# Optimization experiments

Hardware: AMD Instinct MI355X
Metric: run time of the kernel (lower is better)

Reference implementation:

```python
import jax, jax.numpy as jnp
import numpy as np

MARGIN = 0.3
EPS = 1e-16


def _pairwise_distances(e):
    # e: [N, D] -> [N, N] euclidean distances (non-squared path)
    dot = jnp.matmul(e, e.T)
    sq = jnp.diagonal(dot)
    d = sq[None, :] + sq[:, None] - 2.0 * dot
    d = jnp.maximum(d, 0.0)
    zmask = (d == 0.0).astype(d.dtype)
    d = jnp.sqrt(d + zmask * EPS) * (1.0 - zmask)
    return d


def _masks(labels):
    n = labels.shape[0]
    eq = labels[None, :] == labels[:, None]          # [N, N]
    not_diag = ~jnp.eye(n, dtype=bool)
    ap_mask = eq & not_diag                          # anchor-positive
    an_mask = ~eq                                    # anchor-negative
    return ap_mask, an_mask


def _hard_loss(e, labels):
    d = _pairwise_distances(e)
    ap_mask, an_mask = _masks(labels)
    apf = ap_mask.astype(d.dtype)
    anf = an_mask.astype(d.dtype)
    hardest_pos = (apf * d).max(axis=1)
    max_d = d.max()
    hardest_neg = (d + max_d * (1.0 - anf)).min(axis=1)
    tl = jax.nn.relu(hardest_pos - hardest_neg + MARGIN)
    valid = apf.sum(axis=1) > 0
    cnt = valid.sum().astype(d.dtype)
    mean_loss = jnp.where(valid, tl, 0.0).sum() / jnp.maximum(cnt, 1.0)
    return jnp.where(cnt > 0, mean_loss, (e * 0).sum())


def _semi_hard_loss(e, labels):
    d = _pairwise_distances(e)                       # [N, N]
    ap_mask, an_mask = _masks(labels)
    ap = d[:, :, None]                               # [N, N, 1] anchor-positive dist
    an = d[:, None, :]                               # [N, 1, N] anchor-negative dist
    loss = ap - an + MARGIN                          # [N, N, N]
    valid = (ap_mask[:, :, None] & an_mask[:, None, :]
             & (an > ap) & (loss > 0))               # [N, N, N] bool
    num_valid = valid.sum()
    semi = (loss * valid.astype(loss.dtype)).sum() / jnp.maximum(
        num_valid.astype(loss.dtype), 1.0)
    return jnp.where(num_valid > 0, semi, _hard_loss(e, labels))


def setup_inputs() -> dict:
    key = jax.random.key(0)
    k1, k2 = jax.random.split(key)
    embeddings = jax.random.normal(k1, (384, 256), dtype=jnp.float32)
    labels = jax.random.randint(k2, (384,), 0, 32, dtype=jnp.int64)
    return {"embeddings": embeddings, "labels": labels}


def reference(embeddings, labels):
    return _semi_hard_loss(embeddings, labels)
```

## Files before the change

kernel.cpp:

```cpp
#include <hip/hip_runtime.h>
#include <math.h>

#define N 384
#define D 256
#define D4 (D/4)
#define A 3
#define GRID (N/A)
#define TPB N
#define NW (TPB/64)
#define MARGIN_F 0.3f

__global__ __launch_bounds__(TPB) void k_rows(const float* __restrict__ e,
                                              const int* __restrict__ labels,
                                              float* __restrict__ semi_sum,
                                              int* __restrict__ semi_cnt,
                                              float* __restrict__ hp_arr,
                                              float* __restrict__ mn_arr,
                                              float* __restrict__ rm_arr,
                                              int* __restrict__ pc_arr) {
  __shared__ float4 ei[A][D4];
  __shared__ float  nrm[N];
  __shared__ float  row[A][N];
  __shared__ float  negd[A][N];
  __shared__ int    lab[N];
  __shared__ int    poslist[A][N];
  __shared__ int    npos[A];
  __shared__ float  wredf[A][4][NW];
  __shared__ int    wredi[A][2][NW];

  const int b = blockIdx.x;
  const int t = threadIdx.x;
  const int i0 = b * A;

  lab[t] = labels[t];
  if (t < A * D4) {
    int a = t / D4, c = t % D4;
    ei[a][c] = ((const float4*)e)[(size_t)(i0 + a) * D4 + c];
  }
  if (t < A) npos[t] = 0;
  __syncthreads();

  const float4* ej = (const float4*)(e + (size_t)t * D);
  float4 dv0 = {0,0,0,0}, dv1 = {0,0,0,0}, dv2 = {0,0,0,0}, nv = {0,0,0,0};
#pragma unroll 8
  for (int c = 0; c < D4; ++c) {
    float4 v = ej[c];
    nv.x += v.x*v.x; nv.y += v.y*v.y; nv.z += v.z*v.z; nv.w += v.w*v.w;
    float4 u0 = ei[0][c];
    dv0.x += u0.x*v.x; dv0.y += u0.y*v.y; dv0.z += u0.z*v.z; dv0.w += u0.w*v.w;
    float4 u1 = ei[1][c];
    dv1.x += u1.x*v.x; dv1.y += u1.y*v.y; dv1.z += u1.z*v.z; dv1.w += u1.w*v.w;
    float4 u2 = ei[2][c];
    dv2.x += u2.x*v.x; dv2.y += u2.y*v.y; dv2.z += u2.z*v.z; dv2.w += u2.w*v.w;
  }
  const float nj = (nv.x + nv.y) + (nv.z + nv.w);
  float dots[A];
  dots[0] = (dv0.x + dv0.y) + (dv0.z + dv0.w);
  dots[1] = (dv1.x + dv1.y) + (dv1.z + dv1.w);
  dots[2] = (dv2.x + dv2.y) + (dv2.z + dv2.w);
  nrm[t] = nj;
  __syncthreads();

  const int lj = lab[t];
  float hpv[A], mnv[A], rmv[A];
  int   pcv[A];
#pragma unroll
  for (int a = 0; a < A; ++a) {
    const float ni = nrm[i0 + a];
    float d2 = fmaxf(ni + nj - 2.0f * dots[a], 0.0f);
    float dvv = (d2 > 0.0f) ? sqrtf(d2) : 0.0f;
    const bool eq    = (lj == lab[i0 + a]);
    const bool ispos = eq && (t != i0 + a);
    row[a][t]  = dvv;
    negd[a][t] = eq ? 1e30f : dvv;
    rmv[a] = dvv;
    mnv[a] = eq ? 1e30f : dvv;
    hpv[a] = ispos ? dvv : 0.0f;
    pcv[a] = ispos ? 1 : 0;
    if (ispos) { int idx = atomicAdd(&npos[a], 1); poslist[a][idx] = t; }
  }
  __syncthreads();

  const int w = t >> 6;
#pragma unroll
  for (int a = 0; a < A; ++a) {
    const float an = negd[a][t];
    float s = 0.0f;
    int   c = 0;
    const int np = npos[a];
    for (int p = 0; p < np; ++p) {
      const float ap = row[a][poslist[a][p]];
      const float loss = ap - an + MARGIN_F;
      if (an > ap && loss > 0.0f) { s += loss; c++; }
    }
    float hp = hpv[a], mn = mnv[a], rm = rmv[a];
    int   pc = pcv[a];
    for (int off = 32; off; off >>= 1) {
      s  += __shfl_down(s, off);
      c  += __shfl_down(c, off);
      hp  = fmaxf(hp, __shfl_down(hp, off));
      mn  = fminf(mn, __shfl_down(mn, off));
      rm  = fmaxf(rm, __shfl_down(rm, off));
      pc += __shfl_down(pc, off);
    }
    if ((t & 63) == 0) {
      wredf[a][0][w] = s;  wredf[a][1][w] = hp;
      wredf[a][2][w] = mn; wredf[a][3][w] = rm;
      wredi[a][0][w] = c;  wredi[a][1][w] = pc;
    }
  }
  __syncthreads();
  if (t < A) {
    float S = 0.0f, HP = 0.0f, MN = 1e30f, RM = 0.0f;
    int   C = 0, PC = 0;
    for (int ww = 0; ww < NW; ++ww) {
      S += wredf[t][0][ww];
      HP = fmaxf(HP, wredf[t][1][ww]);
      MN = fminf(MN, wredf[t][2][ww]);
      RM = fmaxf(RM, wredf[t][3][ww]);
      C += wredi[t][0][ww];
      PC += wredi[t][1][ww];
    }
    const int i = i0 + t;
    semi_sum[i] = S; semi_cnt[i] = C;
    hp_arr[i] = HP;  mn_arr[i] = MN;
    rm_arr[i] = RM;  pc_arr[i] = PC;
  }
}

__global__ __launch_bounds__(N) void k_final(const float* __restrict__ semi_sum,
                                             const int* __restrict__ semi_cnt,
                                             const float* __restrict__ hp_arr,
                                             const float* __restrict__ mn_arr,
                                             const float* __restrict__ rm_arr,
                                             const int* __restrict__ pc_arr,
                                             float* __restrict__ out) {
  const int t = threadIdx.x;
  __shared__ float shf[12];
  __shared__ int   shi[6];
  __shared__ float s_maxd, s_tsum;
  __shared__ int   s_tcnt;

  float s  = semi_sum[t];
  float rm = rm_arr[t];
  int   c  = semi_cnt[t];
  for (int off = 32; off; off >>= 1) {
    s += __shfl_down(s, off);
    rm = fmaxf(rm, __shfl_down(rm, off));
    c += __shfl_down(c, off);
  }
  const int wv = t >> 6;
  if ((t & 63) == 0) { shf[wv] = s; shf[6 + wv] = rm; shi[wv] = c; }
  __syncthreads();
  if (t == 0) {
    float ts = 0.0f, md = 0.0f; int tc = 0;
    for (int w = 0; w < 6; ++w) { ts += shf[w]; md = fmaxf(md, shf[6 + w]); tc += shi[w]; }
    s_tsum = ts; s_tcnt = tc; s_maxd = md;
  }
  __syncthreads();
  const float maxd = s_maxd;

  float hp  = hp_arr[t];
  float mnv = mn_arr[t];
  int   pcv = pc_arr[t];
  float hn  = fminf(mnv, maxd);
  float tl  = fmaxf(hp - hn + MARGIN_F, 0.0f);
  int   vld = (pcv > 0) ? 1 : 0;
  float contrib = vld ? tl : 0.0f;
  for (int off = 32; off; off >>= 1) {
    contrib += __shfl_down(contrib, off);
    vld += __shfl_down(vld, off);
  }
  __syncthreads();
  if ((t & 63) == 0) { shf[wv] = contrib; shi[wv] = vld; }
  __syncthreads();
  if (t == 0) {
    float hs = 0.0f; int vc = 0;
    for (int w = 0; w < 6; ++w) { hs += shf[w]; vc += shi[w]; }
    float semi = s_tsum / fmaxf((float)s_tcnt, 1.0f);
    float hard = (vc > 0) ? (hs / (float)vc) : 0.0f;
    out[0] = (s_tcnt > 0) ? semi : hard;
  }
}

extern "C" void kernel_launch(void* const* d_in, const int* in_sizes, int n_in,
                              void* d_out, int out_size, void* d_ws, size_t ws_size,
                              hipStream_t stream) {
  (void)in_sizes; (void)n_in; (void)out_size; (void)ws_size;
  const float* e      = (const float*)d_in[0];
  const int*   labels = (const int*)d_in[1];
  float*       out    = (float*)d_out;

  float* ws       = (float*)d_ws;
  float* semi_sum = ws;
  float* hp_arr   = ws + N;
  float* mn_arr   = ws + 2 * N;
  float* rm_arr   = ws + 3 * N;
  int*   semi_cnt = (int*)(ws + 4 * N);
  int*   pc_arr   = (int*)(ws + 5 * N);

  k_rows<<<GRID, TPB, 0, stream>>>(e, labels, semi_sum, semi_cnt,
                                   hp_arr, mn_arr, rm_arr, pc_arr);
  k_final<<<1, N, 0, stream>>>(semi_sum, semi_cnt, hp_arr, mn_arr, rm_arr,
                               pc_arr, out);
}
```

Baseline: 75.34 us.

## Coalesce embedding loads via 16-lane cooperative dot products and single-wave final reduce

In the old row kernel each thread streamed its own embedding row with strided float4 loads, so a wave's accesses were uncoalesced across 64 rows. Now 16 lanes cooperate on one row, each reading contiguous float4 chunks, and combine partial norms and dot products with width-16 shuffles before staging them in shared memory. This is meant to improve global-memory coalescing, at the cost of extra shuffles, a shared-memory round trip and one more barrier. The final kernel also drops from six waves to a single wave that reduces with shuffles only, removing its shared-memory and barrier steps.

After: 70.94 us. -5.8%, faster.

```diff
diff --git a/kernel.cpp b/kernel.cpp
--- a/kernel.cpp
+++ b/kernel.cpp
@@ -20,6 +20,7 @@
                                               int* __restrict__ pc_arr) {
   __shared__ float4 ei[A][D4];
   __shared__ float  nrm[N];
+  __shared__ float  sdot[N][A];
   __shared__ float  row[A][N];
   __shared__ float  negd[A][N];
   __shared__ int    lab[N];
@@ -40,28 +41,47 @@
   if (t < A) npos[t] = 0;
   __syncthreads();
 
-  const float4* ej = (const float4*)(e + (size_t)t * D);
-  float4 dv0 = {0,0,0,0}, dv1 = {0,0,0,0}, dv2 = {0,0,0,0}, nv = {0,0,0,0};
-#pragma unroll 8
-  for (int c = 0; c < D4; ++c) {
-    float4 v = ej[c];
-    nv.x += v.x*v.x; nv.y += v.y*v.y; nv.z += v.z*v.z; nv.w += v.w*v.w;
-    float4 u0 = ei[0][c];
-    dv0.x += u0.x*v.x; dv0.y += u0.y*v.y; dv0.z += u0.z*v.z; dv0.w += u0.w*v.w;
-    float4 u1 = ei[1][c];
-    dv1.x += u1.x*v.x; dv1.y += u1.y*v.y; dv1.z += u1.z*v.z; dv1.w += u1.w*v.w;
-    float4 u2 = ei[2][c];
-    dv2.x += u2.x*v.x; dv2.y += u2.y*v.y; dv2.z += u2.z*v.z; dv2.w += u2.w*v.w;
-  }
-  const float nj = (nv.x + nv.y) + (nv.z + nv.w);
+  {
+    const int w   = t >> 6;
+    const int ln  = t & 63;
+    const int r4  = ln >> 4;
+    const int l16 = ln & 15;
+    const float4* e4 = (const float4*)e;
+    for (int p = 0; p < 16; ++p) {
+      const int j = w * 64 + p * 4 + r4;
+      float nj = 0.f, d0 = 0.f, d1 = 0.f, d2 = 0.f;
+#pragma unroll
+      for (int k = 0; k < 4; ++k) {
+        const int c = l16 + k * 16;
+        const float4 v  = e4[(size_t)j * D4 + c];
+        const float4 u0 = ei[0][c];
+        const float4 u1 = ei[1][c];
+        const float4 u2 = ei[2][c];
+        nj += v.x*v.x + v.y*v.y + v.z*v.z + v.w*v.w;
+        d0 += u0.x*v.x + u0.y*v.y + u0.z*v.z + u0.w*v.w;
+        d1 += u1.x*v.x + u1.y*v.y + u1.z*v.z + u1.w*v.w;
+        d2 += u2.x*v.x + u2.y*v.y + u2.z*v.z + u2.w*v.w;
+      }
+#pragma unroll
+      for (int off = 8; off; off >>= 1) {
+        nj += __shfl_down(nj, off, 16);
+        d0 += __shfl_down(d0, off, 16);
+        d1 += __shfl_down(d1, off, 16);
+        d2 += __shfl_down(d2, off, 16);
+      }
+      if (l16 == 0) {
+        nrm[j] = nj;
+        sdot[j][0] = d0; sdot[j][1] = d1; sdot[j][2] = d2;
+      }
+    }
+  }
+  __syncthreads();
+
+  const int lj = lab[t];
+  const float nj = nrm[t];
   float dots[A];
-  dots[0] = (dv0.x + dv0.y) + (dv0.z + dv0.w);
-  dots[1] = (dv1.x + dv1.y) + (dv1.z + dv1.w);
-  dots[2] = (dv2.x + dv2.y) + (dv2.z + dv2.w);
-  nrm[t] = nj;
-  __syncthreads();
-
-  const int lj = lab[t];
+  dots[0] = sdot[t][0]; dots[1] = sdot[t][1]; dots[2] = sdot[t][2];
+
   float hpv[A], mnv[A], rmv[A];
   int   pcv[A];
 #pragma unroll
@@ -128,58 +148,54 @@
   }
 }
 
-__global__ __launch_bounds__(N) void k_final(const float* __restrict__ semi_sum,
-                                             const int* __restrict__ semi_cnt,
-                                             const float* __restrict__ hp_arr,
-                                             const float* __restrict__ mn_arr,
-                                             const float* __restrict__ rm_arr,
-                                             const int* __restrict__ pc_arr,
-                                             float* __restrict__ out) {
+__global__ __launch_bounds__(64) void k_final(const float* __restrict__ semi_sum,
+                                              const int* __restrict__ semi_cnt,
+                                              const float* __restrict__ hp_arr,
+                                              const float* __restrict__ mn_arr,
+                                              const float* __restrict__ rm_arr,
+                                              const int* __restrict__ pc_arr,
+                                              float* __restrict__ out) {
   const int t = threadIdx.x;
-  __shared__ float shf[12];
-  __shared__ int   shi[6];
-  __shared__ float s_maxd, s_tsum;
-  __shared__ int   s_tcnt;
-
-  float s  = semi_sum[t];
-  float rm = rm_arr[t];
-  int   c  = semi_cnt[t];
+
+  float S = 0.0f, RM = 0.0f;
+  int   C = 0;
+#pragma unroll
+  for (int i = 0; i < 6; ++i) {
+    const int r = t + 64 * i;
+    S += semi_sum[r];
+    RM = fmaxf(RM, rm_arr[r]);
+    C += semi_cnt[r];
+  }
   for (int off = 32; off; off >>= 1) {
-    s += __shfl_down(s, off);
-    rm = fmaxf(rm, __shfl_down(rm, off));
-    c += __shfl_down(c, off);
-  }
-  const int wv = t >> 6;
-  if ((t & 63) == 0) { shf[wv] = s; shf[6 + wv] = rm; shi[wv] = c; }
-  __syncthreads();
+    S  += __shfl_down(S, off);
+    RM  = fmaxf(RM, __shfl_down(RM, off));
+    C  += __shfl_down(C, off);
+  }
+  S  = __shfl(S, 0);
+  RM = __shfl(RM, 0);
+  C  = __shfl(C, 0);
+  const float maxd = RM;
+
+  float hs = 0.0f;
+  int   vc = 0;
+#pragma unroll
+  for (int i = 0; i < 6; ++i) {
+    const int r = t + 64 * i;
+    const float hp = hp_arr[r];
+    const float mn = mn_arr[r];
+    const int   pc = pc_arr[r];
+    const float hn = fminf(mn, maxd);
+    const float tl = fmaxf(hp - hn + MARGIN_F, 0.0f);
+    if (pc > 0) { hs += tl; vc += 1; }
+  }
+  for (int off = 32; off; off >>= 1) {
+    hs += __shfl_down(hs, off);
+    vc += __shfl_down(vc, off);
+  }
   if (t == 0) {
-    float ts = 0.0f, md = 0.0f; int tc = 0;
-    for (int w = 0; w < 6; ++w) { ts += shf[w]; md = fmaxf(md, shf[6 + w]); tc += shi[w]; }
-    s_tsum = ts; s_tcnt = tc; s_maxd = md;
-  }
-  __syncthreads();
-  const float maxd = s_maxd;
-
-  float hp  = hp_arr[t];
-  float mnv = mn_arr[t];
-  int   pcv = pc_arr[t];
-  float hn  = fminf(mnv, maxd);
-  float tl  = fmaxf(hp - hn + MARGIN_F, 0.0f);
-  int   vld = (pcv > 0) ? 1 : 0;
-  float contrib = vld ? tl : 0.0f;
-  for (int off = 32; off; off >>= 1) {
-    contrib += __shfl_down(contrib, off);
-    vld += __shfl_down(vld, off);
-  }
-  __syncthreads();
-  if ((t & 63) == 0) { shf[wv] = contrib; shi[wv] = vld; }
-  __syncthreads();
-  if (t == 0) {
-    float hs = 0.0f; int vc = 0;
-    for (int w = 0; w < 6; ++w) { hs += shf[w]; vc += shi[w]; }
-    float semi = s_tsum / fmaxf((float)s_tcnt, 1.0f);
-    float hard = (vc > 0) ? (hs / (float)vc) : 0.0f;
-    out[0] = (s_tcnt > 0) ? semi : hard;
+    const float semi = S / fmaxf((float)C, 1.0f);
+    const float hard = (vc > 0) ? (hs / (float)vc) : 0.0f;
+    out[0] = (C > 0) ? semi : hard;
   }
 }
 
@@ -201,6 +217,6 @@
 
   k_rows<<<GRID, TPB, 0, stream>>>(e, labels, semi_sum, semi_cnt,
                                    hp_arr, mn_arr, rm_arr, pc_arr);
-  k_final<<<1, N, 0, stream>>>(semi_sum, semi_cnt, hp_arr, mn_arr, rm_arr,
-                               pc_arr, out);
+  k_final<<<1, 64, 0, stream>>>(semi_sum, semi_cnt, hp_arr, mn_arr, rm_arr,
+                                pc_arr, out);
 }
```
